# Performance work log

Hardware: AMD Instinct MI355X
Metric: run time of the kernel (lower is better)

## Reference

```python
import jax, jax.numpy as jnp
import numpy as np

# Keras LSTM gate order: i, f, c(g), o; sigmoid recurrent activation, tanh activation.
# mask_zero=True semantics: at masked steps, h and c carry through unchanged and the
# emitted output equals the previous h (so return_sequences=False yields last valid h).

def _lstm(x, mask, W, U, b):
    # x: [B,S,D], mask: [B,S] bool, W: [D,4H], U: [H,4H], b: [4H]
    B, S, _ = x.shape
    H = U.shape[0]
    xz = jnp.einsum('bsd,dh->bsh', x, W) + b  # precompute input contributions
    h0 = jnp.zeros((B, H), x.dtype)
    c0 = jnp.zeros((B, H), x.dtype)
    def step(carry, inp):
        h, c = carry
        zx, m = inp  # zx: [B,4H], m: [B]
        z = zx + h @ U
        i, f, g, o = jnp.split(z, 4, axis=-1)
        c_new = jax.nn.sigmoid(f) * c + jax.nn.sigmoid(i) * jnp.tanh(g)
        h_new = jax.nn.sigmoid(o) * jnp.tanh(c_new)
        m = m[:, None]
        h = jnp.where(m, h_new, h)
        c = jnp.where(m, c_new, c)
        return (h, c), h
    (hT, _), hs = jax.lax.scan(step, (h0, c0), (jnp.swapaxes(xz, 0, 1), mask.T))
    return jnp.swapaxes(hs, 0, 1), hT  # [B,S,H], [B,H]


def _bilstm(x, mask, Wf, Uf, bf, Wb, Ub, bb, return_seq):
    hs_f, hT_f = _lstm(x, mask, Wf, Uf, bf)
    hs_b, hT_b = _lstm(x[:, ::-1], mask[:, ::-1], Wb, Ub, bb)
    if return_seq:
        return jnp.concatenate([hs_f, hs_b[:, ::-1]], axis=-1)
    return jnp.concatenate([hT_f, hT_b], axis=-1)


def _leaky(x):
    return jnp.where(x >= 0, x, 0.2 * x)  # tf.nn.leaky_relu alpha=0.2


def setup_inputs() -> dict:
    key = jax.random.key(0)
    ks = jax.random.split(key, 32)
    B, S, V, D, H = 64, 256, 32000, 300, 512
    s = 0.05
    inp = {}
    inp['text'] = jax.random.randint(ks[0], (B, S), 0, V)
    inp['emb'] = jax.random.normal(ks[1], (V, D), jnp.float32) * s
    # layer 0: input D, layer 1: input 2H
    inp['W0f'] = jax.random.normal(ks[2], (D, 4 * H), jnp.float32) * s
    inp['U0f'] = jax.random.normal(ks[3], (H, 4 * H), jnp.float32) * s
    inp['b0f'] = jnp.zeros((4 * H,), jnp.float32)
    inp['W0b'] = jax.random.normal(ks[4], (D, 4 * H), jnp.float32) * s
    inp['U0b'] = jax.random.normal(ks[5], (H, 4 * H), jnp.float32) * s
    inp['b0b'] = jnp.zeros((4 * H,), jnp.float32)
    inp['W1f'] = jax.random.normal(ks[6], (2 * H, 4 * H), jnp.float32) * s
    inp['U1f'] = jax.random.normal(ks[7], (H, 4 * H), jnp.float32) * s
    inp['b1f'] = jnp.zeros((4 * H,), jnp.float32)
    inp['W1b'] = jax.random.normal(ks[8], (2 * H, 4 * H), jnp.float32) * s
    inp['U1b'] = jax.random.normal(ks[9], (H, 4 * H), jnp.float32) * s
    inp['b1b'] = jnp.zeros((4 * H,), jnp.float32)
    inp['d0w'] = jax.random.normal(ks[10], (2 * H, 512), jnp.float32) * s
    inp['d0b'] = jnp.zeros((512,), jnp.float32)
    inp['d1w'] = jax.random.normal(ks[11], (512, 256), jnp.float32) * s
    inp['d1b'] = jnp.zeros((256,), jnp.float32)
    inp['d2w'] = jax.random.normal(ks[12], (256, 1), jnp.float32) * s
    inp['d2b'] = jnp.zeros((1,), jnp.float32)
    return inp


def reference(text, emb, W0f, U0f, b0f, W0b, U0b, b0b, W1f, U1f, b1f, W1b, U1b, b1b, d0w, d0b, d1w, d1b, d2w, d2b):
    mask = text != 0  # mask_zero=True
    x = emb[text]  # [B,S,D]
    x = _bilstm(x, mask, W0f, U0f, b0f, W0b, U0b, b0b, return_seq=True)  # [B,S,2H]
    # Dropout is identity at inference (training=False)
    x = _bilstm(x, mask, W1f, U1f, b1f, W1b, U1b, b1b, return_seq=False)  # [B,2H]
    x = _leaky(x @ d0w + d0b)
    x = _leaky(x @ d1w + d1b)
    out = x @ d2w + d2b  # [B,1]
    return out
```

## Files before the change

kernel.cpp:

```cpp
#include <hip/hip_runtime.h>
#include <hip/hip_fp16.h>
#include <math.h>

#define NB   64
#define NS   256
#define ND   300
#define NDP  320
#define NH   512
#define N4H  2048

typedef _Float16 half8_t __attribute__((ext_vector_type(8)));
typedef float    f32x4_t __attribute__((ext_vector_type(4)));

typedef const __attribute__((address_space(1))) unsigned int gas_u32;
typedef __attribute__((address_space(3))) unsigned int las_u32;

__device__ __forceinline__ float fast_sig(float x) {
  return 1.f / (1.f + __expf(-x));
}
__device__ __forceinline__ float fast_tanh(float x) {
  float ax = fabsf(x);
  float e  = __expf(2.f * ax);
  float r  = 1.f - 2.f / (e + 1.f);
  return copysignf(r, x);
}

__global__ void embed_f16_kernel(const int* __restrict__ text,
                                 const float* __restrict__ emb,
                                 _Float16* __restrict__ x) {
  const int bs = blockIdx.x;
  const int tok = text[bs];
  const float* src = emb + (size_t)tok * ND;
  _Float16* dst = x + (size_t)bs * NDP;
  for (int d = threadIdx.x; d < NDP; d += 256)
    dst[d] = (d < ND) ? (_Float16)src[d] : (_Float16)0.f;
}

__global__ __launch_bounds__(256) void gemm_mfma_kernel(
    const _Float16* __restrict__ A, const float* __restrict__ W,
    const float* __restrict__ bias, __half* __restrict__ C,
    int M, int N, int K, int Kw) {
  __shared__ __align__(16) _Float16 as[128][40];
  __shared__ __align__(16) _Float16 ws16[128][40];
  __shared__ __align__(16) float    ws32[32][132];
  const int t = threadIdx.x;
  const int w = t >> 6;
  const int l = t & 63;
  const int lane16 = l & 15;
  const int kq = l >> 4;
  const int bm = blockIdx.y * 128;
  const int bn = blockIdx.x * 128;
  const int lr  = t >> 2;
  const int lsg = t & 3;
  const int wk  = t >> 3;
  const int wns = t & 7;
  const int rn  = t >> 1;
  const int rk0 = (t & 1) * 2;

  f32x4_t acc[2][8];
#pragma unroll
  for (int i = 0; i < 2; i++)
#pragma unroll
    for (int j = 0; j < 8; j++) acc[i][j] = (f32x4_t){0.f, 0.f, 0.f, 0.f};

  for (int k0 = 0; k0 < K; k0 += 32) {
#pragma unroll
    for (int h = 0; h < 2; h++) {
      int m = h * 64 + lr;
      *(uint4*)&as[m][lsg * 8] = *(const uint4*)(A + (size_t)(bm + m) * K + k0 + lsg * 8);
    }
    if (k0 + wk < Kw) {
#pragma unroll
      for (int i = 0; i < 4; i++)
        *(float4*)&ws32[wk][wns * 16 + i * 4] =
            *(const float4*)(W + (size_t)(k0 + wk) * N + bn + wns * 16 + i * 4);
    } else {
#pragma unroll
      for (int i = 0; i < 4; i++)
        *(float4*)&ws32[wk][wns * 16 + i * 4] = make_float4(0.f, 0.f, 0.f, 0.f);
    }
    __syncthreads();
#pragma unroll
    for (int g = 0; g < 2; g++) {
      int kqq = rk0 + g;
      half8_t hv;
#pragma unroll
      for (int jj = 0; jj < 8; jj++) hv[jj] = (_Float16)ws32[kqq * 8 + jj][rn];
      *(half8_t*)&ws16[rn][kqq * 8] = hv;
    }
    __syncthreads();
    half8_t afrag[2];
#pragma unroll
    for (int i = 0; i < 2; i++)
      afrag[i] = *(const half8_t*)&as[w * 32 + i * 16 + lane16][kq * 8];
#pragma unroll
    for (int j = 0; j < 8; j++) {
      half8_t bfrag = *(const half8_t*)&ws16[j * 16 + lane16][kq * 8];
#pragma unroll
      for (int i = 0; i < 2; i++)
        acc[i][j] = __builtin_amdgcn_mfma_f32_16x16x32_f16(afrag[i], bfrag, acc[i][j], 0, 0, 0);
    }
    __syncthreads();
  }
#pragma unroll
  for (int j = 0; j < 8; j++) {
    int col = bn + j * 16 + lane16;
    float bv = bias[col];
#pragma unroll
    for (int i = 0; i < 2; i++) {
      int rbase = bm + w * 32 + i * 16 + kq * 4;
#pragma unroll
      for (int r = 0; r < 4; r++)
        C[(size_t)(rbase + r) * N + col] = __float2half(acc[i][j][r] + bv);
    }
  }
}

__global__ __launch_bounds__(256, 1) void scan_ring_kernel(
    const __half* __restrict__ xzf, const __half* __restrict__ xzb,
    const float* __restrict__ Uf, const float* __restrict__ Ub,
    const int* __restrict__ text,
    __half* ring,
    int* flags, int* abortf,
    float* __restrict__ hT_out) {
  __shared__ __align__(16) _Float16 s_h[16 * 512];
  __shared__ __align__(16) float    s_z[4 * 16 * 20];

  const int t   = threadIdx.x;
  const int b   = blockIdx.x;
  const int grp = b & 7;
  const int dir = grp & 1;
  const int q16 = (grp >> 1) * 16;
  const int cblk = b >> 3;
  const int hc0  = cblk * 16;
  const __half* xz = dir ? xzb : xzf;
  const float* U = dir ? Ub : Uf;
  int* myflags = flags + grp * 32;

  const int w    = t >> 6;
  const int lane = t & 63;
  const int l16  = lane & 15;
  const int quad = lane >> 4;

  int st_off[4];
#pragma unroll
  for (int i = 0; i < 4; i++) {
    int qq = i * 256 + t;
    int lrow = qq >> 6, ch = qq & 63;
    st_off[i] = (q16 + lrow) * (NS * 1024) + ((ch ^ lrow) * 8);
  }
  const __half* ringd = ring + dir * NH;

  const int cc = t & 15, rr = t >> 4;
  const int gr = q16 + rr;
  int xz_off[4];
#pragma unroll
  for (int g = 0; g < 4; g++)
    xz_off[g] = gr * (NS * N4H) + g * NH + hc0 + cc;
  const int t_off = gr * NS;

  half8_t ufrag[16];
  {
    const int col = w * NH + hc0 + l16;
#pragma unroll
    for (int kt = 0; kt < 16; kt++)
#pragma unroll
      for (int jj = 0; jj < 8; jj++)
        ufrag[kt][jj] = (_Float16)U[(size_t)(kt * 32 + quad * 8 + jj) * N4H + col];
  }

  float c_st = 0.f, h_st = 0.f;
  __half xzrA[4], xzrB[4];
  int tmA, tmB;
  {
    const int t0 = dir ? (NS - 1) : 0;
    const int t1 = dir ? (NS - 2) : 1;
#pragma unroll
    for (int g = 0; g < 4; g++) xzrA[g] = xz[(size_t)t0 * N4H + xz_off[g]];
    tmA = text[t_off + t0];
#pragma unroll
    for (int g = 0; g < 4; g++) xzrB[g] = xz[(size_t)t1 * N4H + xz_off[g]];
    tmB = text[t_off + t1];
  }

  for (int s = 0; s < NS; s++) {
    const int tt = dir ? (NS - 1 - s) : s;
    f32x4_t acc = {0.f, 0.f, 0.f, 0.f};

    if (s > 0) {
      const int ttp = dir ? (tt + 1) : (tt - 1);
      const __half* srcb = ringd + (size_t)ttp * 1024;
#pragma unroll
      for (int i = 0; i < 4; i++)
        __builtin_amdgcn_global_load_lds((gas_u32*)(srcb + st_off[i]),
                                         (las_u32*)(s_h + (size_t)(i * 256 + t) * 8),
                                         16, 0, 0);
      __syncthreads();
#pragma unroll
      for (int kt = 0; kt < 16; kt++) {
        half8_t af = *(const half8_t*)(s_h + l16 * 512 + (((kt * 4 + quad)) ^ l16) * 8);
        acc = __builtin_amdgcn_mfma_f32_16x16x32_f16(af, ufrag[kt], acc, 0, 0, 0);
      }
    }

    *(f32x4_t*)&s_z[w * 320 + l16 * 20 + quad * 4] = acc;
    __syncthreads();

    {
      __half x0, x1, x2, x3; int tmsk;
      if ((s & 1) == 0) { x0 = xzrA[0]; x1 = xzrA[1]; x2 = xzrA[2]; x3 = xzrA[3]; tmsk = tmA; }
      else              { x0 = xzrB[0]; x1 = xzrB[1]; x2 = xzrB[2]; x3 = xzrB[3]; tmsk = tmB; }
      float zi = s_z[0 * 320 + cc * 20 + rr] + __half2float(x0);
      float zf = s_z[1 * 320 + cc * 20 + rr] + __half2float(x1);
      float zg = s_z[2 * 320 + cc * 20 + rr] + __half2float(x2);
      float zo = s_z[3 * 320 + cc * 20 + rr] + __half2float(x3);
      float ig = fast_sig(zi);
      float fg = fast_sig(zf);
      float gv = fast_tanh(zg);
      float og = fast_sig(zo);
      float cn = fg * c_st + ig * gv;
      float hn = og * fast_tanh(cn);
      if (tmsk != 0) { c_st = cn; h_st = hn; }
      ring[((size_t)gr * NS + tt) * 1024 + dir * NH + hc0 + cc] = __float2half(h_st);
      if (hT_out && s == NS - 1)
        hT_out[(size_t)gr * 1024 + dir * NH + hc0 + cc] = h_st;
    }

    if (s < NS - 1) {
      __syncthreads();
      if (t == 0)
        __hip_atomic_store(myflags + cblk, s + 1, __ATOMIC_RELAXED,
                           __HIP_MEMORY_SCOPE_AGENT);
      if (s + 2 < NS) {
        const int tt2 = dir ? (tt - 2) : (tt + 2);
        if ((s & 1) == 0) {
#pragma unroll
          for (int g = 0; g < 4; g++) xzrA[g] = xz[(size_t)tt2 * N4H + xz_off[g]];
          tmA = text[t_off + tt2];
        } else {
#pragma unroll
          for (int g = 0; g < 4; g++) xzrB[g] = xz[(size_t)tt2 * N4H + xz_off[g]];
          tmB = text[t_off + tt2];
        }
      }
      {
        int aborted = 0, it = 0;
        while (true) {
          int f = __hip_atomic_load(myflags + (lane & 31),
                                    __ATOMIC_RELAXED, __HIP_MEMORY_SCOPE_AGENT);
          if (__all(f >= s + 1)) break;
          __builtin_amdgcn_s_sleep(2);
          if (((++it) & 1023) == 0) {
            if (it > 200000)
              __hip_atomic_store(abortf, 1, __ATOMIC_RELAXED, __HIP_MEMORY_SCOPE_AGENT);
            if (__hip_atomic_load(abortf, __ATOMIC_RELAXED, __HIP_MEMORY_SCOPE_AGENT)) {
              aborted = 1; break;
            }
          }
        }
        if (aborted) return;
      }
    }
  }
}

template <int ACT>
__global__ __launch_bounds__(256) void gemm_kernel(
    const float* __restrict__ A, const float* __restrict__ W,
    const float* __restrict__ bias, float* __restrict__ C,
    int M, int N, int K) {
  __shared__ __align__(16) float As[8][128];
  __shared__ __align__(16) float Bs[8][128];
  const int t  = threadIdx.x;
  const int bn = blockIdx.x * 128;
  const int bm = blockIdx.y * 128;
  const int tx = t & 15, ty = t >> 4;
  const int lm  = t >> 1;
  const int lk4 = (t & 1) * 4;
  const int lbk = t >> 5;
  const int lbn = (t & 31) * 4;
  float acc[8][8];
#pragma unroll
  for (int i = 0; i < 8; i++)
#pragma unroll
    for (int j = 0; j < 8; j++) acc[i][j] = 0.f;

  for (int k0 = 0; k0 < K; k0 += 8) {
#pragma unroll
    for (int i = 0; i < 4; i++) {
      int k = k0 + lk4 + i;
      int m = bm + lm;
      float v = 0.f;
      if (k < K && m < M) v = A[(size_t)m * K + k];
      As[lk4 + i][lm] = v;
    }
    {
      int k = k0 + lbk;
      float4 v = make_float4(0.f, 0.f, 0.f, 0.f);
      if (k < K) v = *(const float4*)(W + (size_t)k * N + bn + lbn);
      *(float4*)(&Bs[lbk][lbn]) = v;
    }
    __syncthreads();
#pragma unroll
    for (int kk = 0; kk < 8; kk++) {
      float a[8], bb[8];
      *(float4*)(a)      = *(const float4*)(&As[kk][ty * 8]);
      *(float4*)(a + 4)  = *(const float4*)(&As[kk][ty * 8 + 4]);
      *(float4*)(bb)     = *(const float4*)(&Bs[kk][tx * 8]);
      *(float4*)(bb + 4) = *(const float4*)(&Bs[kk][tx * 8 + 4]);
#pragma unroll
      for (int i = 0; i < 8; i++)
#pragma unroll
        for (int j = 0; j < 8; j++) acc[i][j] += a[i] * bb[j];
    }
    __syncthreads();
  }
  float4 bv0 = *(const float4*)(bias + bn + tx * 8);
  float4 bv1 = *(const float4*)(bias + bn + tx * 8 + 4);
#pragma unroll
  for (int i = 0; i < 8; i++) {
    int m = bm + ty * 8 + i;
    if (m >= M) continue;
    float4 o0, o1;
    o0.x = acc[i][0] + bv0.x; o0.y = acc[i][1] + bv0.y;
    o0.z = acc[i][2] + bv0.z; o0.w = acc[i][3] + bv0.w;
    o1.x = acc[i][4] + bv1.x; o1.y = acc[i][5] + bv1.y;
    o1.z = acc[i][6] + bv1.z; o1.w = acc[i][7] + bv1.w;
    if (ACT == 1) {
      o0.x = o0.x >= 0.f ? o0.x : 0.2f * o0.x;  o0.y = o0.y >= 0.f ? o0.y : 0.2f * o0.y;
      o0.z = o0.z >= 0.f ? o0.z : 0.2f * o0.z;  o0.w = o0.w >= 0.f ? o0.w : 0.2f * o0.w;
      o1.x = o1.x >= 0.f ? o1.x : 0.2f * o1.x;  o1.y = o1.y >= 0.f ? o1.y : 0.2f * o1.y;
      o1.z = o1.z >= 0.f ? o1.z : 0.2f * o1.z;  o1.w = o1.w >= 0.f ? o1.w : 0.2f * o1.w;
    }
    *(float4*)(C + (size_t)m * N + bn + tx * 8)     = o0;
    *(float4*)(C + (size_t)m * N + bn + tx * 8 + 4) = o1;
  }
}

__global__ void final_kernel(const float* __restrict__ a1, const float* __restrict__ w,
                             const float* __restrict__ bias, float* __restrict__ out) {
  const int b = blockIdx.x, t = threadIdx.x;
  float v = a1[b * 256 + t] * w[t];
#pragma unroll
  for (int off = 32; off > 0; off >>= 1) v += __shfl_down(v, off, 64);
  __shared__ float red[4];
  if ((t & 63) == 0) red[t >> 6] = v;
  __syncthreads();
  if (t == 0) out[b] = (red[0] + red[1]) + (red[2] + red[3]) + bias[0];
}

extern "C" void kernel_launch(void* const* d_in, const int* in_sizes, int n_in,
                              void* d_out, int out_size, void* d_ws, size_t ws_size,
                              hipStream_t stream) {
  const int*   text = (const int*)  d_in[0];
  const float* emb  = (const float*)d_in[1];
  const float* W0f  = (const float*)d_in[2];
  const float* U0f  = (const float*)d_in[3];
  const float* b0f  = (const float*)d_in[4];
  const float* W0b  = (const float*)d_in[5];
  const float* U0b  = (const float*)d_in[6];
  const float* b0b  = (const float*)d_in[7];
  const float* W1f  = (const float*)d_in[8];
  const float* U1f  = (const float*)d_in[9];
  const float* b1f  = (const float*)d_in[10];
  const float* W1b  = (const float*)d_in[11];
  const float* U1b  = (const float*)d_in[12];
  const float* b1b  = (const float*)d_in[13];
  const float* d0w  = (const float*)d_in[14];
  const float* d0b  = (const float*)d_in[15];
  const float* d1w  = (const float*)d_in[16];
  const float* d1b  = (const float*)d_in[17];
  const float* d2w  = (const float*)d_in[18];
  const float* d2b  = (const float*)d_in[19];
  float* out = (float*)d_out;

  char* p = (char*)d_ws;
  __half* xzA = (__half*)p;  p += (size_t)NB * NS * N4H * 2;
  __half* xzB = (__half*)p;  p += (size_t)NB * NS * N4H * 2;
  char* region1 = p;         p += (size_t)NB * NS * 1024 * 2;
  _Float16* x_emb = (_Float16*)region1;
  __half*   hs0   = (__half*)region1;
  __half* hp0  = (__half*)p;  p += 64 * 1024 * 2;
  __half* hp1  = (__half*)p;  p += 64 * 1024 * 2;
  int*    cnt  = (int*)p;     p += 64 * 1024 * 4;
  float*  feat = (float*)p;   p += 64 * 1024 * 4;
  float*  a0   = (float*)p;   p += 64 * 512 * 4;
  float*  a1   = (float*)p;   p += 64 * 256 * 4;
  (void)hp0; (void)hp1;
  int* flags0 = cnt;
  int* flags1 = cnt + 256;
  int* abortf = cnt + 512;

  hipMemsetAsync(cnt, 0, 516 * sizeof(int), stream);
  hipLaunchKernelGGL(embed_f16_kernel, dim3(NB * NS), dim3(256), 0, stream, text, emb, x_emb);

  dim3 gmf(16, 128);
  hipLaunchKernelGGL(gemm_mfma_kernel, gmf, dim3(256), 0, stream, x_emb, W0f, b0f, xzA, 16384, N4H, NDP, ND);
  hipLaunchKernelGGL(gemm_mfma_kernel, gmf, dim3(256), 0, stream, x_emb, W0b, b0b, xzB, 16384, N4H, NDP, ND);

  hipLaunchKernelGGL(scan_ring_kernel, dim3(256), dim3(256), 0, stream,
                     xzA, xzB, U0f, U0b, text, hs0, flags0, abortf, (float*)nullptr);

  hipLaunchKernelGGL(gemm_mfma_kernel, gmf, dim3(256), 0, stream, (const _Float16*)hs0, W1f, b1f, xzA, 16384, N4H, 1024, 1024);
  hipLaunchKernelGGL(gemm_mfma_kernel, gmf, dim3(256), 0, stream, (const _Float16*)hs0, W1b, b1b, xzB, 16384, N4H, 1024, 1024);

  hipLaunchKernelGGL(scan_ring_kernel, dim3(256), dim3(256), 0, stream,
                     xzA, xzB, U1f, U1b, text, hs0, flags1, abortf, feat);

  gemm_kernel<1><<<dim3(4, 1), dim3(256), 0, stream>>>(feat, d0w, d0b, a0, 64, 512, 1024);
  gemm_kernel<1><<<dim3(2, 1), dim3(256), 0, stream>>>(a0, d1w, d1b, a1, 64, 256, 512);
  hipLaunchKernelGGL(final_kernel, dim3(64), dim3(256), 0, stream, a1, d2w, d2b, out);
}
```

Baseline: 2.220 ms.

## Pre-transpose input weights to fp16 and use LDS-direct-load MFMA GEMM

Adds a kernel that transposes and converts each input-projection weight matrix to fp16 in N-major layout once per call. A new GEMM kernel then loads both A and the transposed weights straight into LDS with global_load_lds and an XOR swizzle, avoiding the fp32 weight staging and in-kernel conversion. This costs extra transpose launches and workspace, and falls back to the old GEMM if the workspace is too small. The recurrent scans, which likely dominate runtime, are unchanged.

Result: faster. 2.093 ms (-5.7%).

```diff
diff --git a/kernel.cpp b/kernel.cpp
--- a/kernel.cpp
+++ b/kernel.cpp
@@ -34,6 +34,89 @@
   _Float16* dst = x + (size_t)bs * NDP;
   for (int d = threadIdx.x; d < NDP; d += 256)
     dst[d] = (d < ND) ? (_Float16)src[d] : (_Float16)0.f;
+}
+
+__global__ __launch_bounds__(256) void wtrans_kernel(
+    const float* __restrict__ W, _Float16* __restrict__ Wt, int Kw, int Kp) {
+  __shared__ float tile[64][65];
+  const int n0 = blockIdx.x * 64, k0 = blockIdx.y * 64;
+  const int tn = threadIdx.x & 63, tg = threadIdx.x >> 6;
+#pragma unroll
+  for (int i = 0; i < 16; i++) {
+    int k = k0 + tg * 16 + i;
+    tile[tg * 16 + i][tn] = (k < Kw) ? W[(size_t)k * 2048 + n0 + tn] : 0.f;
+  }
+  __syncthreads();
+#pragma unroll
+  for (int i = 0; i < 16; i++) {
+    int n = n0 + tg * 16 + i;
+    Wt[(size_t)n * Kp + k0 + tn] = (_Float16)tile[tn][tg * 16 + i];
+  }
+}
+
+__global__ __launch_bounds__(256) void gemm_mfma_v3_kernel(
+    const _Float16* __restrict__ A, const _Float16* __restrict__ Wt,
+    const float* __restrict__ bias, __half* __restrict__ C,
+    int M, int N, int K) {
+  __shared__ __align__(16) _Float16 s_a[128 * 32];
+  __shared__ __align__(16) _Float16 s_w[128 * 32];
+  const int t = threadIdx.x;
+  const int w = t >> 6;
+  const int l = t & 63;
+  const int lane16 = l & 15;
+  const int kq = l >> 4;
+  const int bm = blockIdx.y * 128;
+  const int bn = blockIdx.x * 128;
+
+  f32x4_t acc[2][8];
+#pragma unroll
+  for (int i = 0; i < 2; i++)
+#pragma unroll
+    for (int j = 0; j < 8; j++) acc[i][j] = (f32x4_t){0.f, 0.f, 0.f, 0.f};
+
+  for (int k0 = 0; k0 < K; k0 += 32) {
+#pragma unroll
+    for (int i = 0; i < 2; i++) {
+      int lchunk = i * 256 + t;
+      int row = lchunk >> 2;
+      int cq  = lchunk & 3;
+      int koff = (cq ^ ((row >> 1) & 3)) * 8;
+      __builtin_amdgcn_global_load_lds(
+          (gas_u32*)(A + (size_t)(bm + row) * K + k0 + koff),
+          (las_u32*)(s_a + (size_t)lchunk * 8), 16, 0, 0);
+      __builtin_amdgcn_global_load_lds(
+          (gas_u32*)(Wt + (size_t)(bn + row) * K + k0 + koff),
+          (las_u32*)(s_w + (size_t)lchunk * 8), 16, 0, 0);
+    }
+    __syncthreads();
+    half8_t afrag[2];
+#pragma unroll
+    for (int i = 0; i < 2; i++) {
+      int row = w * 32 + i * 16 + lane16;
+      afrag[i] = *(const half8_t*)(s_a + row * 32 + (kq ^ ((row >> 1) & 3)) * 8);
+    }
+#pragma unroll
+    for (int j = 0; j < 8; j++) {
+      int col = j * 16 + lane16;
+      half8_t bfrag = *(const half8_t*)(s_w + col * 32 + (kq ^ ((col >> 1) & 3)) * 8);
+#pragma unroll
+      for (int i = 0; i < 2; i++)
+        acc[i][j] = __builtin_amdgcn_mfma_f32_16x16x32_f16(afrag[i], bfrag, acc[i][j], 0, 0, 0);
+    }
+    __syncthreads();
+  }
+#pragma unroll
+  for (int j = 0; j < 8; j++) {
+    int col = bn + j * 16 + lane16;
+    float bv = bias[col];
+#pragma unroll
+    for (int i = 0; i < 2; i++) {
+      int rbase = bm + w * 32 + i * 16 + kq * 4;
+#pragma unroll
+      for (int r = 0; r < 4; r++)
+        C[(size_t)(rbase + r) * N + col] = __float2half(acc[i][j][r] + bv);
+    }
+  }
 }
 
 __global__ __launch_bounds__(256) void gemm_mfma_kernel(
@@ -391,18 +474,49 @@
   int* flags1 = cnt + 256;
   int* abortf = cnt + 512;
 
+  uintptr_t pa = ((uintptr_t)p + 15) & ~(uintptr_t)15;
+  size_t used = (size_t)(pa - (uintptr_t)d_ws);
+  const size_t wt0_bytes = (size_t)2048 * NDP * 2;
+  const size_t wt1_bytes = (size_t)2048 * 1024 * 2;
+  const size_t wt_total  = 2 * wt0_bytes + 2 * wt1_bytes;
+  const bool use_wt = (ws_size >= used + wt_total);
+  _Float16 *wt0f = nullptr, *wt0b = nullptr, *wt1f = nullptr, *wt1b = nullptr;
+  if (use_wt) {
+    char* q = (char*)pa;
+    wt0f = (_Float16*)q; q += wt0_bytes;
+    wt0b = (_Float16*)q; q += wt0_bytes;
+    wt1f = (_Float16*)q; q += wt1_bytes;
+    wt1b = (_Float16*)q; q += wt1_bytes;
+  }
+
   hipMemsetAsync(cnt, 0, 516 * sizeof(int), stream);
+  if (use_wt) {
+    hipLaunchKernelGGL(wtrans_kernel, dim3(32, NDP / 64), dim3(256), 0, stream, W0f, wt0f, ND, NDP);
+    hipLaunchKernelGGL(wtrans_kernel, dim3(32, NDP / 64), dim3(256), 0, stream, W0b, wt0b, ND, NDP);
+    hipLaunchKernelGGL(wtrans_kernel, dim3(32, 1024 / 64), dim3(256), 0, stream, W1f, wt1f, 1024, 1024);
+    hipLaunchKernelGGL(wtrans_kernel, dim3(32, 1024 / 64), dim3(256), 0, stream, W1b, wt1b, 1024, 1024);
+  }
   hipLaunchKernelGGL(embed_f16_kernel, dim3(NB * NS), dim3(256), 0, stream, text, emb, x_emb);
 
   dim3 gmf(16, 128);
-  hipLaunchKernelGGL(gemm_mfma_kernel, gmf, dim3(256), 0, stream, x_emb, W0f, b0f, xzA, 16384, N4H, NDP, ND);
-  hipLaunchKernelGGL(gemm_mfma_kernel, gmf, dim3(256), 0, stream, x_emb, W0b, b0b, xzB, 16384, N4H, NDP, ND);
+  if (use_wt) {
+    hipLaunchKernelGGL(gemm_mfma_v3_kernel, gmf, dim3(256), 0, stream, x_emb, wt0f, b0f, xzA, 16384, N4H, NDP);
+    hipLaunchKernelGGL(gemm_mfma_v3_kernel, gmf, dim3(256), 0, stream, x_emb, wt0b, b0b, xzB, 16384, N4H, NDP);
+  } else {
+    hipLaunchKernelGGL(gemm_mfma_kernel, gmf, dim3(256), 0, stream, x_emb, W0f, b0f, xzA, 16384, N4H, NDP, ND);
+    hipLaunchKernelGGL(gemm_mfma_kernel, gmf, dim3(256), 0, stream, x_emb, W0b, b0b, xzB, 16384, N4H, NDP, ND);
+  }
 
   hipLaunchKernelGGL(scan_ring_kernel, dim3(256), dim3(256), 0, stream,
                      xzA, xzB, U0f, U0b, text, hs0, flags0, abortf, (float*)nullptr);
 
-  hipLaunchKernelGGL(gemm_mfma_kernel, gmf, dim3(256), 0, stream, (const _Float16*)hs0, W1f, b1f, xzA, 16384, N4H, 1024, 1024);
-  hipLaunchKernelGGL(gemm_mfma_kernel, gmf, dim3(256), 0, stream, (const _Float16*)hs0, W1b, b1b, xzB, 16384, N4H, 1024, 1024);
+  if (use_wt) {
+    hipLaunchKernelGGL(gemm_mfma_v3_kernel, gmf, dim3(256), 0, stream, (const _Float16*)hs0, wt1f, b1f, xzA, 16384, N4H, 1024);
+    hipLaunchKernelGGL(gemm_mfma_v3_kernel, gmf, dim3(256), 0, stream, (const _Float16*)hs0, wt1b, b1b, xzB, 16384, N4H, 1024);
+  } else {
+    hipLaunchKernelGGL(gemm_mfma_kernel, gmf, dim3(256), 0, stream, (const _Float16*)hs0, W1f, b1f, xzA, 16384, N4H, 1024, 1024);
+    hipLaunchKernelGGL(gemm_mfma_kernel, gmf, dim3(256), 0, stream, (const _Float16*)hs0, W1b, b1b, xzB, 16384, N4H, 1024, 1024);
+  }
 
   hipLaunchKernelGGL(scan_ring_kernel, dim3(256), dim3(256), 0, stream,
                      xzA, xzB, U1f, U1b, text, hs0, flags1, abortf, feat);
```
